# Optimization experiments

Measured on AMD Instinct MI355X. Metric: run time of the kernel, lower is better.

Reference implementation:

```python
import jax, jax.numpy as jnp
import numpy as np

B, N, C = 16, 1024, 768
E, H, D, K = 8, 192, 4, 2


def setup_inputs() -> dict:
    key = jax.random.key(0)
    ks = jax.random.split(key, 8)
    std = 0.02
    return {
        "x": jax.random.normal(ks[0], (B, N, C), jnp.float32),
        "task_ids": jax.random.randint(ks[1], (B,), 0, D),
        "eps": jax.random.normal(ks[2], (B, N, E), jnp.float32),
        "gate_w": jax.random.normal(ks[3], (D, C, 2 * E), jnp.float32) * std,
        "fc1_w": jax.random.normal(ks[4], (E, H, C), jnp.float32) * std,
        "fc1_b": jnp.zeros((E, H), jnp.float32),
        "fc2_w": jax.random.normal(ks[5], (E, C, H), jnp.float32) * std,
        "fc2_b": jnp.zeros((E, C), jnp.float32),
    }


def reference(x, task_ids, eps, gate_w, fc1_w, fc1_b, fc2_w, fc2_b):
    # per-sample gate selected by domain/task id: [B,N,2E]
    total_w = jnp.einsum("bnc,bce->bne", x, gate_w[task_ids])
    clean_logits, raw_noise = jnp.split(total_w, 2, axis=-1)  # [B,N,E] each
    noise_stddev = jax.nn.softplus(raw_noise) + 0.01
    logits = clean_logits + eps * noise_stddev  # [B,N,E]
    exp_wise_sum = logits.sum(axis=1)  # [B,E]

    top_k_logits, top_k_idx = jax.lax.top_k(exp_wise_sum, K)  # [B,K]
    m1 = top_k_logits.min(axis=1, keepdims=True)
    m2 = top_k_logits.max(axis=1, keepdims=True)
    scaled = (top_k_logits - m1) / (m2 - m1 + 1e-6)
    top_k_gates = jax.nn.softmax(scaled, axis=1)  # [B,K]

    gates_full = jnp.zeros((B, E), x.dtype).at[
        jnp.arange(B)[:, None], top_k_idx
    ].set(top_k_gates)  # [B,E]

    # dense all-expert adapter compute (faithful to original torch.stack)
    h = jnp.einsum("bnc,ehc->benh", x, fc1_w) + fc1_b[None, :, None, :]
    h = jax.nn.gelu(h, approximate=False)
    expert_outs = jnp.einsum("benh,ech->benc", h, fc2_w) + fc2_b[None, :, None, :]

    tot_x = jnp.einsum("be,benc->bnc", gates_full, expert_outs)
    return x + tot_x
```

## Files before the change

### kernel.cpp

```cpp
#include <hip/hip_runtime.h>

#define B_ 16
#define N_ 1024
#define C_ 768
#define E_ 8
#define H_ 192
#define K_ 2

typedef __bf16 bf16x8 __attribute__((ext_vector_type(8)));
typedef float  f32x4  __attribute__((ext_vector_type(4)));

__global__ __launch_bounds__(256) void prep_kernel(
    const float* __restrict__ w1, const float* __restrict__ w2,
    const float* __restrict__ gw,
    __bf16* __restrict__ pw1, __bf16* __restrict__ pw2,
    float* __restrict__ gwT) {
  int idx = blockIdx.x * 256 + threadIdx.x;
  const int nW4 = (E_ * H_ * C_) / 4;
  if (idx >= nW4) return;
  int flat = idx * 4;
  int e = flat / (H_ * C_);
  int r = flat - e * (H_ * C_);

  {
    float4 a = *(const float4*)(w1 + (size_t)flat);
    int n = r / C_;
    int c = r - n * C_;
    size_t o = ((size_t)(e * 24 + (c >> 5)) * 192 + n) * 32 + (c & 31);
    pw1[o + 0] = (__bf16)a.x; pw1[o + 1] = (__bf16)a.y;
    pw1[o + 2] = (__bf16)a.z; pw1[o + 3] = (__bf16)a.w;
  }
  {
    float4 a = *(const float4*)(w2 + (size_t)flat);
    int n = r / H_;
    int h = r - n * H_;
    size_t o = ((size_t)(e * 6 + (h >> 5)) * 768 + n) * 32 + (h & 31);
    pw2[o + 0] = (__bf16)a.x; pw2[o + 1] = (__bf16)a.y;
    pw2[o + 2] = (__bf16)a.z; pw2[o + 3] = (__bf16)a.w;
  }
  if (idx < (4 * 16 * C_) / 4) {
    int f = idx * 4;
    int d = f / (16 * C_);
    int rr = f - d * (16 * C_);
    int j = rr / C_;
    int c = rr - j * C_;
    const float* src = gw + (size_t)d * C_ * 16 + j;
    float4 v;
    v.x = src[(size_t)(c + 0) * 16]; v.y = src[(size_t)(c + 1) * 16];
    v.z = src[(size_t)(c + 2) * 16]; v.w = src[(size_t)(c + 3) * 16];
    *(float4*)(gwT + (size_t)f) = v;
  }
}

__global__ __launch_bounds__(256, 3) void gate_kernel(
    const float* __restrict__ x, const int* __restrict__ task_ids,
    const float* __restrict__ eps, const float* __restrict__ gwT,
    float* __restrict__ sums) {
  const int b = blockIdx.x >> 6;
  const int token0 = (blockIdx.x & 63) * 16;
  const int tid = threadIdx.x;

  __shared__ __align__(16) float xt[16][772];
  __shared__ float sc[16][16];
  __shared__ float red[16][8];

  const float* xbase = x + ((size_t)b * N_ + token0) * C_;
  for (int it = 0; it < 12; ++it) {
    int chunk = it * 256 + tid;
    int row = chunk / 192;
    int col4 = chunk - row * 192;
    float4 v = *(const float4*)(xbase + (size_t)row * C_ + col4 * 4);
    *(float4*)&xt[row][col4 * 4] = v;
  }
  __syncthreads();

  const int t = tid & 15;
  const int j = tid >> 4;
  const int task = task_ids[b];
  const float* wrow = gwT + ((size_t)task * 16 + j) * C_;
  float acc = 0.0f;
#pragma unroll 4
  for (int c = 0; c < C_; c += 4) {
    float4 xv = *(const float4*)&xt[t][c];
    float4 wv = *(const float4*)(wrow + c);
    acc += xv.x * wv.x + xv.y * wv.y + xv.z * wv.z + xv.w * wv.w;
  }
  sc[t][j] = acc;
  __syncthreads();
  if (j < 8) {
    float clean = sc[t][j];
    float raw = sc[t][j + 8];
    float sp = (raw > 20.0f) ? raw : log1pf(expf(raw));
    float lg = clean + eps[((size_t)b * N_ + token0 + t) * E_ + j] * (sp + 0.01f);
    red[t][j] = lg;
  }
  __syncthreads();
  if (tid < 8) {
    float s = 0.0f;
#pragma unroll
    for (int tt = 0; tt < 16; ++tt) s += red[tt][tid];
    atomicAdd(&sums[b * E_ + tid], s);
  }
}

__global__ __launch_bounds__(256, 2) void expert_kernel(
    const float* __restrict__ x, const __bf16* __restrict__ pw1,
    const __bf16* __restrict__ pw2, const float* __restrict__ fc1_b,
    const float* __restrict__ fc2_b, const float* __restrict__ sums,
    float* __restrict__ out) {
  const int b = blockIdx.x >> 5;
  const int token0 = (blockIdx.x & 31) * 32;
  const int tid = threadIdx.x;
  const int wave = tid >> 6;
  const int lane = tid & 63;
  const int ln = lane & 15;
  const int q8 = (lane >> 4) * 8;
  const int q4 = (lane >> 4) * 4;

  __shared__ __align__(16) __bf16 xs[32][776];
  __shared__ __align__(16) __bf16 hs[32][200];

  int e_idx[2]; float gate_v[2];
  {
    const float* s = sums + b * E_;
    float best = -INFINITY, best2 = -INFINITY;
    int i1 = 0, i2 = 0;
#pragma unroll
    for (int e = 0; e < E_; ++e) {
      float v = s[e];
      if (v > best) { best2 = best; i2 = i1; best = v; i1 = e; }
      else if (v > best2) { best2 = v; i2 = e; }
    }
    float d = best - best2;
    float st = d / (d + 1e-6f);
    float et = expf(st);
    e_idx[0] = i1; gate_v[0] = et / (et + 1.0f);
    e_idx[1] = i2; gate_v[1] = 1.0f / (et + 1.0f);
  }

  const float* xbase = x + ((size_t)b * N_ + token0) * C_;
  for (int it = 0; it < 12; ++it) {
    int chunk = it * 256 + tid;
    int row = chunk / 96;
    int col8 = chunk - row * 96;
    const float* p = xbase + (size_t)row * C_ + col8 * 8;
    float4 v0 = *(const float4*)p;
    float4 v1 = *(const float4*)(p + 4);
    bf16x8 t;
    t[0] = (__bf16)v0.x; t[1] = (__bf16)v0.y; t[2] = (__bf16)v0.z; t[3] = (__bf16)v0.w;
    t[4] = (__bf16)v1.x; t[5] = (__bf16)v1.y; t[6] = (__bf16)v1.z; t[7] = (__bf16)v1.w;
    *(bf16x8*)&xs[row][col8 * 8] = t;
  }
  __syncthreads();

  f32x4 c2[2][12] = {};

  for (int kx = 0; kx < 2; ++kx) {
    const int e = e_idx[kx];
    const float g = gate_v[kx];

    const __bf16* w1l = pw1 + (size_t)e * (24 * 192 * 32)
                            + (size_t)(wave * 48 + ln) * 32 + q8;
    bf16x8 bq[2][3], aq[2][2];
#pragma unroll
    for (int j = 0; j < 3; ++j) bq[0][j] = *(const bf16x8*)(w1l + j * 512);
    aq[0][0] = *(const bf16x8*)&xs[ln][q8];
    aq[0][1] = *(const bf16x8*)&xs[16 + ln][q8];
    f32x4 c1[2][3] = {};
#pragma unroll
    for (int kb = 0; kb < 24; ++kb) {
      int p = kb & 1;
      if (kb < 23) {
        const __bf16* nx = w1l + (size_t)(kb + 1) * 6144;
#pragma unroll
        for (int j = 0; j < 3; ++j) bq[p ^ 1][j] = *(const bf16x8*)(nx + j * 512);
        aq[p ^ 1][0] = *(const bf16x8*)&xs[ln][(kb + 1) * 32 + q8];
        aq[p ^ 1][1] = *(const bf16x8*)&xs[16 + ln][(kb + 1) * 32 + q8];
      }
#pragma unroll
      for (int j = 0; j < 3; ++j) {
        c1[0][j] = __builtin_amdgcn_mfma_f32_16x16x32_bf16(aq[p][0], bq[p][j], c1[0][j], 0, 0, 0);
        c1[1][j] = __builtin_amdgcn_mfma_f32_16x16x32_bf16(aq[p][1], bq[p][j], c1[1][j], 0, 0, 0);
      }
    }
#pragma unroll
    for (int j = 0; j < 3; ++j) {
      int col = wave * 48 + j * 16 + ln;
      float b1 = fc1_b[e * H_ + col];
#pragma unroll
      for (int m = 0; m < 2; ++m) {
#pragma unroll
        for (int r = 0; r < 4; ++r) {
          int row = m * 16 + q4 + r;
          float v = c1[m][j][r] + b1;
          float gl = 0.5f * v * (1.0f + erff(v * 0.70710678118f));
          hs[row][col] = (__bf16)(g * gl);
        }
      }
    }
    __syncthreads();

    const __bf16* w2l = pw2 + (size_t)e * (6 * 768 * 32)
                            + (size_t)(wave * 192 + ln) * 32 + q8;
    bf16x8 bh[2][6], av[2][2];
#pragma unroll
    for (int j = 0; j < 6; ++j) bh[0][j] = *(const bf16x8*)(w2l + j * 512);
    av[0][0] = *(const bf16x8*)&hs[ln][q8];
    av[0][1] = *(const bf16x8*)&hs[16 + ln][q8];
#pragma unroll
    for (int s = 0; s < 12; ++s) {
      const int kb = s >> 1;
      const int half = s & 1;
      const int p = s & 1;
      if (s < 11) {
        const int s2 = s + 1;
        const int kb2 = s2 >> 1;
        const int half2 = s2 & 1;
        const __bf16* src = w2l + (size_t)kb2 * 24576;
#pragma unroll
        for (int j = 0; j < 6; ++j)
          bh[p ^ 1][j] = *(const bf16x8*)(src + (half2 * 6 + j) * 512);
        if (half2 == 0) {
          av[kb2 & 1][0] = *(const bf16x8*)&hs[ln][kb2 * 32 + q8];
          av[kb2 & 1][1] = *(const bf16x8*)&hs[16 + ln][kb2 * 32 + q8];
        }
      }
#pragma unroll
      for (int j = 0; j < 6; ++j) {
        const int jj = half * 6 + j;
        c2[0][jj] = __builtin_amdgcn_mfma_f32_16x16x32_bf16(av[kb & 1][0], bh[p][j], c2[0][jj], 0, 0, 0);
        c2[1][jj] = __builtin_amdgcn_mfma_f32_16x16x32_bf16(av[kb & 1][1], bh[p][j], c2[1][jj], 0, 0, 0);
      }
    }
    __syncthreads();
  }

  const float* xr = x + ((size_t)b * N_ + token0) * C_;
  float* outr = out + ((size_t)b * N_ + token0) * C_;
#pragma unroll
  for (int j = 0; j < 12; ++j) {
    int col = wave * 192 + j * 16 + ln;
    float b2t = gate_v[0] * fc2_b[e_idx[0] * C_ + col] +
                gate_v[1] * fc2_b[e_idx[1] * C_ + col];
#pragma unroll
    for (int m = 0; m < 2; ++m) {
#pragma unroll
      for (int r = 0; r < 4; ++r) {
        int row = m * 16 + q4 + r;
        size_t off = (size_t)row * C_ + col;
        outr[off] = xr[off] + c2[m][j][r] + b2t;
      }
    }
  }
}

extern "C" void kernel_launch(void* const* d_in, const int* in_sizes, int n_in,
                              void* d_out, int out_size, void* d_ws, size_t ws_size,
                              hipStream_t stream) {
  const float* x      = (const float*)d_in[0];
  const int*   task   = (const int*)d_in[1];
  const float* eps    = (const float*)d_in[2];
  const float* gate_w = (const float*)d_in[3];
  const float* fc1_w  = (const float*)d_in[4];
  const float* fc1_b  = (const float*)d_in[5];
  const float* fc2_w  = (const float*)d_in[6];
  const float* fc2_b  = (const float*)d_in[7];
  float* out = (float*)d_out;

  const size_t nW = (size_t)E_ * H_ * C_;
  __bf16* pw1 = (__bf16*)d_ws;
  __bf16* pw2 = pw1 + nW;
  float* gwT  = (float*)((char*)d_ws + 2 * nW * sizeof(__bf16));
  float* sums = (float*)((char*)gwT + 4 * 16 * C_ * sizeof(float));

  hipMemsetAsync(sums, 0, B_ * E_ * sizeof(float), stream);
  prep_kernel<<<(nW / 4 + 255) / 256, 256, 0, stream>>>(fc1_w, fc2_w, gate_w,
                                                        pw1, pw2, gwT);
  gate_kernel<<<B_ * 64, 256, 0, stream>>>(x, task, eps, gwT, sums);
  expert_kernel<<<B_ * 32, 256, 0, stream>>>(x, pw1, pw2, fc1_b, fc2_b,
                                             sums, out);
}
```

Before: 207.5 us.

## Factor clean-logit sum via column sums; enlarge expert tiles to 64 tokens

The gate kernel now computes only the noise-half dot products and accumulates per-batch column sums of x, so the token-summed clean logits come from a single xsum·W dot product inside the expert kernel. This uses the linearity of the sum over tokens to halve the per-token gate work. The expert kernel moves to 512-thread blocks covering 64 tokens with a 2x4 wave grid, triple-buffered register prefetch and dynamic shared memory, and remaps blocks to spread batches. The trade-offs are extra atomics on xsum, larger shared memory per block and a different floating-point summation order for the gate.

```diff
diff --git a/kernel.cpp b/kernel.cpp
--- a/kernel.cpp
+++ b/kernel.cpp
@@ -55,7 +55,7 @@
 __global__ __launch_bounds__(256, 3) void gate_kernel(
     const float* __restrict__ x, const int* __restrict__ task_ids,
     const float* __restrict__ eps, const float* __restrict__ gwT,
-    float* __restrict__ sums) {
+    float* __restrict__ sums, float* __restrict__ xsum) {
   const int b = blockIdx.x >> 6;
   const int token0 = (blockIdx.x & 63) * 16;
   const int tid = threadIdx.x;
@@ -76,23 +76,35 @@
 
   const int t = tid & 15;
   const int j = tid >> 4;
+  const int e = j & 7;
+  const int half = j >> 3;
   const int task = task_ids[b];
-  const float* wrow = gwT + ((size_t)task * 16 + j) * C_;
+  const float* wrow = gwT + ((size_t)task * 16 + 8 + e) * C_ + half * 384;
+  const float* xrow = &xt[t][half * 384];
   float acc = 0.0f;
 #pragma unroll 4
-  for (int c = 0; c < C_; c += 4) {
-    float4 xv = *(const float4*)&xt[t][c];
+  for (int c = 0; c < 384; c += 4) {
+    float4 xv = *(const float4*)(xrow + c);
     float4 wv = *(const float4*)(wrow + c);
     acc += xv.x * wv.x + xv.y * wv.y + xv.z * wv.z + xv.w * wv.w;
   }
   sc[t][j] = acc;
+
+#pragma unroll
+  for (int cc = 0; cc < 3; ++cc) {
+    int col = tid * 3 + cc;
+    float s = 0.0f;
+#pragma unroll
+    for (int tt = 0; tt < 16; ++tt) s += xt[tt][col];
+    atomicAdd(&xsum[(size_t)b * C_ + col], s);
+  }
   __syncthreads();
-  if (j < 8) {
-    float clean = sc[t][j];
-    float raw = sc[t][j + 8];
+
+  if (tid < 128) {
+    int t2 = tid & 15, e2 = tid >> 4;
+    float raw = sc[t2][e2] + sc[t2][e2 + 8];
     float sp = (raw > 20.0f) ? raw : log1pf(expf(raw));
-    float lg = clean + eps[((size_t)b * N_ + token0 + t) * E_ + j] * (sp + 0.01f);
-    red[t][j] = lg;
+    red[t2][e2] = eps[((size_t)b * N_ + token0 + t2) * E_ + e2] * (sp + 0.01f);
   }
   __syncthreads();
   if (tid < 8) {
@@ -103,31 +115,70 @@
   }
 }
 
-__global__ __launch_bounds__(256, 2) void expert_kernel(
+#define SMEM_EXPERT (64 * 776 * 2 + 64 * 200 * 2 + 32)
+
+__global__ __launch_bounds__(512, 2) void expert_kernel(
     const float* __restrict__ x, const __bf16* __restrict__ pw1,
     const __bf16* __restrict__ pw2, const float* __restrict__ fc1_b,
     const float* __restrict__ fc2_b, const float* __restrict__ sums,
-    float* __restrict__ out) {
-  const int b = blockIdx.x >> 5;
-  const int token0 = (blockIdx.x & 31) * 32;
+    const float* __restrict__ xsum, const float* __restrict__ gwT,
+    const int* __restrict__ task_ids, float* __restrict__ out) {
+  const int bid = blockIdx.x;
+  const int sxc = bid >> 3;
+  const int b = (bid & 7) * 2 + (sxc >> 4);
+  const int token0 = (sxc & 15) * 64;
   const int tid = threadIdx.x;
   const int wave = tid >> 6;
+  const int wm = wave >> 2;
+  const int wn = wave & 3;
   const int lane = tid & 63;
   const int ln = lane & 15;
   const int q8 = (lane >> 4) * 8;
   const int q4 = (lane >> 4) * 4;
-
-  __shared__ __align__(16) __bf16 xs[32][776];
-  __shared__ __align__(16) __bf16 hs[32][200];
+  const int arow = wm * 32;
+
+  extern __shared__ char smem[];
+  __bf16 (*xs)[776] = reinterpret_cast<__bf16(*)[776]>(smem);
+  __bf16 (*hs)[200] = reinterpret_cast<__bf16(*)[200]>(smem + 99328);
+  float* sm_clean = reinterpret_cast<float*>(smem + 99328 + 25600);
+
+  const float* xbase = x + ((size_t)b * N_ + token0) * C_;
+  for (int it = 0; it < 12; ++it) {
+    int chunk = it * 512 + tid;
+    int row = chunk / 96;
+    int col8 = chunk - row * 96;
+    const float* p = xbase + (size_t)row * C_ + col8 * 8;
+    float4 v0 = *(const float4*)p;
+    float4 v1 = *(const float4*)(p + 4);
+    bf16x8 tv;
+    tv[0] = (__bf16)v0.x; tv[1] = (__bf16)v0.y; tv[2] = (__bf16)v0.z; tv[3] = (__bf16)v0.w;
+    tv[4] = (__bf16)v1.x; tv[5] = (__bf16)v1.y; tv[6] = (__bf16)v1.z; tv[7] = (__bf16)v1.w;
+    *(bf16x8*)&xs[row][col8 * 8] = tv;
+  }
+
+  {
+    const int task = task_ids[b];
+    const float* xsb = xsum + (size_t)b * C_;
+    const float* gr = gwT + ((size_t)task * 16 + wave) * C_;
+    float cl = 0.0f;
+#pragma unroll
+    for (int c0 = 0; c0 < C_ / 64; ++c0) {
+      int c = c0 * 64 + lane;
+      cl += xsb[c] * gr[c];
+    }
+#pragma unroll
+    for (int off = 32; off; off >>= 1) cl += __shfl_down(cl, off);
+    if (lane == 0) sm_clean[wave] = cl + sums[b * E_ + wave];
+  }
+  __syncthreads();
 
   int e_idx[2]; float gate_v[2];
   {
-    const float* s = sums + b * E_;
     float best = -INFINITY, best2 = -INFINITY;
     int i1 = 0, i2 = 0;
 #pragma unroll
     for (int e = 0; e < E_; ++e) {
-      float v = s[e];
+      float v = sm_clean[e];
       if (v > best) { best2 = best; i2 = i1; best = v; i1 = e; }
       else if (v > best2) { best2 = v; i2 = e; }
     }
@@ -138,21 +189,6 @@
     e_idx[1] = i2; gate_v[1] = 1.0f / (et + 1.0f);
   }
 
-  const float* xbase = x + ((size_t)b * N_ + token0) * C_;
-  for (int it = 0; it < 12; ++it) {
-    int chunk = it * 256 + tid;
-    int row = chunk / 96;
-    int col8 = chunk - row * 96;
-    const float* p = xbase + (size_t)row * C_ + col8 * 8;
-    float4 v0 = *(const float4*)p;
-    float4 v1 = *(const float4*)(p + 4);
-    bf16x8 t;
-    t[0] = (__bf16)v0.x; t[1] = (__bf16)v0.y; t[2] = (__bf16)v0.z; t[3] = (__bf16)v0.w;
-    t[4] = (__bf16)v1.x; t[5] = (__bf16)v1.y; t[6] = (__bf16)v1.z; t[7] = (__bf16)v1.w;
-    *(bf16x8*)&xs[row][col8 * 8] = t;
-  }
-  __syncthreads();
-
   f32x4 c2[2][12] = {};
 
   for (int kx = 0; kx < 2; ++kx) {
@@ -160,39 +196,44 @@
     const float g = gate_v[kx];
 
     const __bf16* w1l = pw1 + (size_t)e * (24 * 192 * 32)
-                            + (size_t)(wave * 48 + ln) * 32 + q8;
-    bf16x8 bq[2][3], aq[2][2];
-#pragma unroll
-    for (int j = 0; j < 3; ++j) bq[0][j] = *(const bf16x8*)(w1l + j * 512);
-    aq[0][0] = *(const bf16x8*)&xs[ln][q8];
-    aq[0][1] = *(const bf16x8*)&xs[16 + ln][q8];
+                            + (size_t)(wn * 48 + ln) * 32 + q8;
+    bf16x8 bq[3][3], aq[3][2];
+#pragma unroll
+    for (int k0 = 0; k0 < 2; ++k0) {
+      const __bf16* nx = w1l + (size_t)k0 * 6144;
+#pragma unroll
+      for (int jj = 0; jj < 3; ++jj) bq[k0][jj] = *(const bf16x8*)(nx + jj * 512);
+      aq[k0][0] = *(const bf16x8*)&xs[arow + ln][k0 * 32 + q8];
+      aq[k0][1] = *(const bf16x8*)&xs[arow + 16 + ln][k0 * 32 + q8];
+    }
     f32x4 c1[2][3] = {};
 #pragma unroll
     for (int kb = 0; kb < 24; ++kb) {
-      int p = kb & 1;
-      if (kb < 23) {
-        const __bf16* nx = w1l + (size_t)(kb + 1) * 6144;
-#pragma unroll
-        for (int j = 0; j < 3; ++j) bq[p ^ 1][j] = *(const bf16x8*)(nx + j * 512);
-        aq[p ^ 1][0] = *(const bf16x8*)&xs[ln][(kb + 1) * 32 + q8];
-        aq[p ^ 1][1] = *(const bf16x8*)&xs[16 + ln][(kb + 1) * 32 + q8];
-      }
-#pragma unroll
-      for (int j = 0; j < 3; ++j) {
-        c1[0][j] = __builtin_amdgcn_mfma_f32_16x16x32_bf16(aq[p][0], bq[p][j], c1[0][j], 0, 0, 0);
-        c1[1][j] = __builtin_amdgcn_mfma_f32_16x16x32_bf16(aq[p][1], bq[p][j], c1[1][j], 0, 0, 0);
-      }
-    }
-#pragma unroll
-    for (int j = 0; j < 3; ++j) {
-      int col = wave * 48 + j * 16 + ln;
+      const int p = kb % 3;
+      if (kb < 22) {
+        const int kn = kb + 2, pn = kn % 3;
+        const __bf16* nx = w1l + (size_t)kn * 6144;
+#pragma unroll
+        for (int jj = 0; jj < 3; ++jj) bq[pn][jj] = *(const bf16x8*)(nx + jj * 512);
+        aq[pn][0] = *(const bf16x8*)&xs[arow + ln][kn * 32 + q8];
+        aq[pn][1] = *(const bf16x8*)&xs[arow + 16 + ln][kn * 32 + q8];
+      }
+#pragma unroll
+      for (int jj = 0; jj < 3; ++jj) {
+        c1[0][jj] = __builtin_amdgcn_mfma_f32_16x16x32_bf16(aq[p][0], bq[p][jj], c1[0][jj], 0, 0, 0);
+        c1[1][jj] = __builtin_amdgcn_mfma_f32_16x16x32_bf16(aq[p][1], bq[p][jj], c1[1][jj], 0, 0, 0);
+      }
+    }
+#pragma unroll
+    for (int jj = 0; jj < 3; ++jj) {
+      int col = wn * 48 + jj * 16 + ln;
       float b1 = fc1_b[e * H_ + col];
 #pragma unroll
       for (int m = 0; m < 2; ++m) {
 #pragma unroll
         for (int r = 0; r < 4; ++r) {
-          int row = m * 16 + q4 + r;
-          float v = c1[m][j][r] + b1;
+          int row = arow + m * 16 + q4 + r;
+          float v = c1[m][jj][r] + b1;
           float gl = 0.5f * v * (1.0f + erff(v * 0.70710678118f));
           hs[row][col] = (__bf16)(g * gl);
         }
@@ -201,35 +242,38 @@
     __syncthreads();
 
     const __bf16* w2l = pw2 + (size_t)e * (6 * 768 * 32)
-                            + (size_t)(wave * 192 + ln) * 32 + q8;
-    bf16x8 bh[2][6], av[2][2];
-#pragma unroll
-    for (int j = 0; j < 6; ++j) bh[0][j] = *(const bf16x8*)(w2l + j * 512);
-    av[0][0] = *(const bf16x8*)&hs[ln][q8];
-    av[0][1] = *(const bf16x8*)&hs[16 + ln][q8];
-#pragma unroll
-    for (int s = 0; s < 12; ++s) {
-      const int kb = s >> 1;
-      const int half = s & 1;
-      const int p = s & 1;
-      if (s < 11) {
-        const int s2 = s + 1;
-        const int kb2 = s2 >> 1;
-        const int half2 = s2 & 1;
+                            + (size_t)(wn * 192 + ln) * 32 + q8;
+    bf16x8 bh[3][6], av[2][2];
+#pragma unroll
+    for (int s0 = 0; s0 < 2; ++s0) {
+#pragma unroll
+      for (int jj = 0; jj < 6; ++jj)
+        bh[s0][jj] = *(const bf16x8*)(w2l + (s0 * 6 + jj) * 512);
+    }
+    av[0][0] = *(const bf16x8*)&hs[arow + ln][q8];
+    av[0][1] = *(const bf16x8*)&hs[arow + 16 + ln][q8];
+#pragma unroll
+    for (int st = 0; st < 12; ++st) {
+      const int kb = st >> 1;
+      const int half = st & 1;
+      const int p = st % 3;
+      if (st < 10) {
+        const int s2 = st + 2;
+        const int kb2 = s2 >> 1, half2 = s2 & 1, p2 = s2 % 3;
         const __bf16* src = w2l + (size_t)kb2 * 24576;
 #pragma unroll
-        for (int j = 0; j < 6; ++j)
-          bh[p ^ 1][j] = *(const bf16x8*)(src + (half2 * 6 + j) * 512);
+        for (int jj = 0; jj < 6; ++jj)
+          bh[p2][jj] = *(const bf16x8*)(src + (half2 * 6 + jj) * 512);
         if (half2 == 0) {
-          av[kb2 & 1][0] = *(const bf16x8*)&hs[ln][kb2 * 32 + q8];
-          av[kb2 & 1][1] = *(const bf16x8*)&hs[16 + ln][kb2 * 32 + q8];
+          av[kb2 & 1][0] = *(const bf16x8*)&hs[arow + ln][kb2 * 32 + q8];
+          av[kb2 & 1][1] = *(const bf16x8*)&hs[arow + 16 + ln][kb2 * 32 + q8];
         }
       }
 #pragma unroll
-      for (int j = 0; j < 6; ++j) {
-        const int jj = half * 6 + j;
-        c2[0][jj] = __builtin_amdgcn_mfma_f32_16x16x32_bf16(av[kb & 1][0], bh[p][j], c2[0][jj], 0, 0, 0);
-        c2[1][jj] = __builtin_amdgcn_mfma_f32_16x16x32_bf16(av[kb & 1][1], bh[p][j], c2[1][jj], 0, 0, 0);
+      for (int jj = 0; jj < 6; ++jj) {
+        const int cj = half * 6 + jj;
+        c2[0][cj] = __builtin_amdgcn_mfma_f32_16x16x32_bf16(av[kb & 1][0], bh[p][jj], c2[0][cj], 0, 0, 0);
+        c2[1][cj] = __builtin_amdgcn_mfma_f32_16x16x32_bf16(av[kb & 1][1], bh[p][jj], c2[1][cj], 0, 0, 0);
       }
     }
     __syncthreads();
@@ -238,17 +282,17 @@
   const float* xr = x + ((size_t)b * N_ + token0) * C_;
   float* outr = out + ((size_t)b * N_ + token0) * C_;
 #pragma unroll
-  for (int j = 0; j < 12; ++j) {
-    int col = wave * 192 + j * 16 + ln;
+  for (int jj = 0; jj < 12; ++jj) {
+    int col = wn * 192 + jj * 16 + ln;
     float b2t = gate_v[0] * fc2_b[e_idx[0] * C_ + col] +
                 gate_v[1] * fc2_b[e_idx[1] * C_ + col];
 #pragma unroll
     for (int m = 0; m < 2; ++m) {
 #pragma unroll
       for (int r = 0; r < 4; ++r) {
-        int row = m * 16 + q4 + r;
+        int row = arow + m * 16 + q4 + r;
         size_t off = (size_t)row * C_ + col;
-        outr[off] = xr[off] + c2[m][j][r] + b2t;
+        outr[off] = xr[off] + c2[m][jj][r] + b2t;
       }
     }
   }
@@ -271,12 +315,16 @@
   __bf16* pw1 = (__bf16*)d_ws;
   __bf16* pw2 = pw1 + nW;
   float* gwT  = (float*)((char*)d_ws + 2 * nW * sizeof(__bf16));
-  float* sums = (float*)((char*)gwT + 4 * 16 * C_ * sizeof(float));
-
-  hipMemsetAsync(sums, 0, B_ * E_ * sizeof(float), stream);
+  float* sums = gwT + 4 * 16 * C_;
+  float* xsum = sums + B_ * E_;
+
+  hipMemsetAsync(sums, 0, (B_ * E_ + B_ * C_) * sizeof(float), stream);
   prep_kernel<<<(nW / 4 + 255) / 256, 256, 0, stream>>>(fc1_w, fc2_w, gate_w,
                                                         pw1, pw2, gwT);
-  gate_kernel<<<B_ * 64, 256, 0, stream>>>(x, task, eps, gwT, sums);
-  expert_kernel<<<B_ * 32, 256, 0, stream>>>(x, pw1, pw2, fc1_b, fc2_b,
-                                             sums, out);
+  gate_kernel<<<B_ * 64, 256, 0, stream>>>(x, task, eps, gwT, sums, xsum);
+
+  hipFuncSetAttribute(reinterpret_cast<const void*>(expert_kernel),
+                      hipFuncAttributeMaxDynamicSharedMemorySize, SMEM_EXPERT);
+  expert_kernel<<<B_ * 16, 512, SMEM_EXPERT, stream>>>(
+      x, pw1, pw2, fc1_b, fc2_b, sums, xsum, gwT, task, out);
 }
```

After: 210.0 us. Within noise of the previous version (+1.2%).
